# Optimization experiments

Measured on AMD Instinct MI355X. Metric: run time of the kernel, lower is better.

## Reference

```python
import jax, jax.numpy as jnp
import numpy as np

DIM = 2048
N_HEADS = 16
KV_HEADS = 2
HEAD_DIM = DIM // N_HEADS
N_REP = N_HEADS // KV_HEADS
EPS = 1e-6


def rms_norm(x, weight):
    # norm over last dim in float32, cast back (inputs already fp32 here)
    xf = x.astype(jnp.float32)
    n = xf * jax.lax.rsqrt(jnp.mean(xf * xf, axis=-1, keepdims=True) + EPS)
    return (weight * n).astype(x.dtype)


def rotate_half(x):
    x1, x2 = jnp.split(x, 2, axis=-1)
    return jnp.concatenate((-x2, x1), axis=-1)


def apply_rotary(x, cos, sin):
    return x * cos + rotate_half(x) * sin


def setup_inputs() -> dict:
    key = jax.random.key(0)
    ks = jax.random.split(key, 8)
    B, S = 2, 2048
    x = jax.random.normal(ks[0], (B, S, DIM), dtype=jnp.float32)
    cos = jax.random.uniform(ks[1], (1, 1, S, HEAD_DIM), dtype=jnp.float32)
    sin = jax.random.uniform(ks[2], (1, 1, S, HEAD_DIM), dtype=jnp.float32)
    scale = 0.02
    wq = jax.random.normal(ks[3], (N_HEADS * HEAD_DIM, DIM), dtype=jnp.float32) * scale
    wk = jax.random.normal(ks[4], (KV_HEADS * HEAD_DIM, DIM), dtype=jnp.float32) * scale
    wv = jax.random.normal(ks[5], (KV_HEADS * HEAD_DIM, DIM), dtype=jnp.float32) * scale
    wo = jax.random.normal(ks[6], (DIM, N_HEADS * HEAD_DIM), dtype=jnp.float32) * scale
    q_gamma = jnp.ones((HEAD_DIM,), dtype=jnp.float32)
    k_gamma = jnp.ones((HEAD_DIM,), dtype=jnp.float32)
    return {"x": x, "cos": cos, "sin": sin, "wq": wq, "wk": wk, "wv": wv,
            "wo": wo, "q_gamma": q_gamma, "k_gamma": k_gamma,
            "signal_token_num": 256}


def reference(x, cos, sin, wq, wk, wv, wo, q_gamma, k_gamma, signal_token_num):
    B, S, D = x.shape
    p = signal_token_num
    # projections (Linear with no bias: x @ W.T)
    xq = (x @ wq.T).reshape(B, S, N_HEADS, HEAD_DIM)
    xk = (x @ wk.T).reshape(B, S, KV_HEADS, HEAD_DIM)
    xv = (x @ wv.T).reshape(B, S, KV_HEADS, HEAD_DIM)
    # QK RMSNorm per head_dim
    xq = rms_norm(xq, q_gamma)
    xk = rms_norm(xk, k_gamma)
    # repeat kv heads (GQA) then [B,H,S,hd]
    xk = jnp.repeat(xk, N_REP, axis=2)
    xv = jnp.repeat(xv, N_REP, axis=2)
    xq = xq.transpose(0, 2, 1, 3)
    xk = xk.transpose(0, 2, 1, 3)
    xv = xv.transpose(0, 2, 1, 3)
    # rotary: original applies identical cos/sin to [:p] and [p:] slices == full apply
    xq = apply_rotary(xq, cos, sin)
    xk = apply_rotary(xk, cos, sin)
    # causal mask with bidirectional prefix block [:p,:p]
    i = jnp.arange(S)[:, None]
    j = jnp.arange(S)[None, :]
    mask = (j <= i) | ((i < p) & (j < p))  # [S,S] bool
    scale = 1.0 / np.sqrt(HEAD_DIM)
    scores = jnp.einsum('bhqd,bhkd->bhqk', xq, xk) * scale
    scores = jnp.where(mask, scores, jnp.finfo(scores.dtype).min)
    attn = jax.nn.softmax(scores, axis=-1)
    out = jnp.einsum('bhqk,bhkd->bhqd', attn, xv)  # [B,H,S,hd]
    out = out.transpose(0, 2, 1, 3).reshape(B, S, N_HEADS * HEAD_DIM)
    return out @ wo.T
```

## Files before the change

### kernel.cpp

```cpp
#include <hip/hip_runtime.h>
#include <stdint.h>

#define S_LEN 2048
#define DIMM  2048
#define NH    16
#define NKV   2

typedef __attribute__((ext_vector_type(8)))  short s16x8;
typedef __attribute__((ext_vector_type(8)))  unsigned short u16x8;
typedef __attribute__((ext_vector_type(4)))  float f32x4;
typedef __attribute__((ext_vector_type(16))) float f32x16;
typedef __attribute__((ext_vector_type(4)))  unsigned int u32x4;

__device__ __forceinline__ unsigned short f2bf(float f){
  unsigned int u = __builtin_bit_cast(unsigned int, f);
  u += 0x7fffu + ((u >> 16) & 1u);
  return (unsigned short)(u >> 16);
}

__device__ __forceinline__ float bf2f(unsigned short u){
  return __builtin_bit_cast(float, ((unsigned int)u) << 16);
}

__device__ __forceinline__ unsigned int cvtpk(float lo, float hi){
  unsigned int r;
  asm("v_cvt_pk_bf16_f32 %0, %1, %2" : "=v"(r) : "v"(lo), "v"(hi));
  return r;
}

__device__ __forceinline__ void gload16(const void* g, void* l){
  __builtin_amdgcn_global_load_lds(
      (const __attribute__((address_space(1))) unsigned int*)g,
      (__attribute__((address_space(3))) unsigned int*)l, 16, 0, 0);
}

__global__ __launch_bounds__(256) void cvt_all(const float* __restrict__ x,
    const float* __restrict__ wq, const float* __restrict__ wk,
    const float* __restrict__ wv, const float* __restrict__ wo,
    unsigned short* __restrict__ xb, unsigned short* __restrict__ wqkvb,
    unsigned short* __restrict__ wob){
  long gid = (long)blockIdx.x * 256 + threadIdx.x;
  const float* src; unsigned short* dst; long off;
  if (gid < 1048576)      { src = x;  dst = xb;              off = gid; }
  else if (gid < 1572864) { src = wq; dst = wqkvb;           off = gid - 1048576; }
  else if (gid < 1638400) { src = wk; dst = wqkvb + 4194304; off = gid - 1572864; }
  else if (gid < 1703936) { src = wv; dst = wqkvb + 4718592; off = gid - 1638400; }
  else                    { src = wo; dst = wob;             off = gid - 1703936; }
  long i = off * 8;
  const float4* s4 = (const float4*)(src + i);
  float4 a = s4[0], b = s4[1];
  u16x8 o;
  o[0]=f2bf(a.x); o[1]=f2bf(a.y); o[2]=f2bf(a.z); o[3]=f2bf(a.w);
  o[4]=f2bf(b.x); o[5]=f2bf(b.y); o[6]=f2bf(b.z); o[7]=f2bf(b.w);
  *(u16x8*)(dst + i) = o;
}

template<bool OBF16>
__global__ __launch_bounds__(256) void gemm_bt(const unsigned short* __restrict__ A,
                                               const unsigned short* __restrict__ W,
                                               void* __restrict__ Cv,
                                               int M, int N, int K){
  __shared__ __attribute__((aligned(16))) unsigned short As[128*64];
  __shared__ __attribute__((aligned(16))) unsigned short Bs[128*64];
  const int t = threadIdx.x;
  const int lane = t & 63, wave = t >> 6;
  const int l15 = lane & 15, g = lane >> 4;
  const int lid = blockIdx.y * gridDim.x + blockIdx.x;
  const int cpx = (gridDim.x * gridDim.y) >> 3;
  const int swz = (lid & 7) * cpx + (lid >> 3);
  const int m0 = (swz / gridDim.x) * 128, n0 = (swz % gridDim.x) * 128;
  const int wm = (wave >> 1) * 64, wn = (wave & 1) * 64;
  const int srow = t >> 3, sdblk = t & 7;
  const long ldsoff = (long)(t >> 6) * 1024;
  f32x4 acc[4][4] = {};
  for (int k0 = 0; k0 < K; k0 += 64){
    __syncthreads();
    #pragma unroll
    for (int r = 0; r < 4; ++r){
      int row = r*32 + srow;
      int db  = sdblk ^ (row & 7);
      gload16(A + (long)(m0+row)*K + k0 + db*8, (char*)As + r*4096 + ldsoff);
    }
    #pragma unroll
    for (int r = 0; r < 4; ++r){
      int row = r*32 + srow;
      int db  = sdblk ^ (row & 7);
      gload16(W + (long)(n0+row)*K + k0 + db*8, (char*)Bs + r*4096 + ldsoff);
    }
    __syncthreads();
    s16x8 af[4][2], bfr[4][2];
    #pragma unroll
    for (int mi = 0; mi < 4; ++mi)
      #pragma unroll
      for (int kc = 0; kc < 2; ++kc){
        int row = wm + mi*16 + l15;
        int db = (kc*4 + g) ^ (row & 7);
        af[mi][kc] = *(const s16x8*)(As + row*64 + db*8);
      }
    #pragma unroll
    for (int ni = 0; ni < 4; ++ni)
      #pragma unroll
      for (int kc = 0; kc < 2; ++kc){
        int row = wn + ni*16 + l15;
        int db = (kc*4 + g) ^ (row & 7);
        bfr[ni][kc] = *(const s16x8*)(Bs + row*64 + db*8);
      }
    #pragma unroll
    for (int mi = 0; mi < 4; ++mi)
      #pragma unroll
      for (int ni = 0; ni < 4; ++ni)
        #pragma unroll
        for (int kc = 0; kc < 2; ++kc)
          acc[mi][ni] = __builtin_amdgcn_mfma_f32_16x16x32_bf16(af[mi][kc], bfr[ni][kc], acc[mi][ni], 0, 0, 0);
  }
  #pragma unroll
  for (int mi = 0; mi < 4; ++mi)
    #pragma unroll
    for (int ni = 0; ni < 4; ++ni)
      #pragma unroll
      for (int rg = 0; rg < 4; ++rg){
        int row = m0 + wm + mi*16 + g*4 + rg;
        int col = n0 + wn + ni*16 + l15;
        if (OBF16)
          ((unsigned short*)Cv)[(long)row*N + col] = f2bf(acc[mi][ni][rg]);
        else
          ((float*)Cv)[(long)row*N + col] = acc[mi][ni][rg];
      }
}

__global__ __launch_bounds__(256) void normrope(const unsigned short* __restrict__ qkv,
    const float* __restrict__ cosb, const float* __restrict__ sinb,
    const float* __restrict__ qg, const float* __restrict__ kg,
    unsigned short* __restrict__ q_attn, unsigned short* __restrict__ k_attn){
  int wave = threadIdx.x >> 6, lane = threadIdx.x & 63;
  int rid = blockIdx.x * 4 + wave;
  int d0 = lane * 2;
  const unsigned short* src; unsigned short* dst; const float* gm; float sc; int s;
  if (rid < 2*S_LEN*NH){
    int bs = rid >> 4, h = rid & 15;
    int b = bs >> 11; s = bs & 2047;
    src = qkv + (long)bs*2560 + h*128;
    dst = q_attn + ((long)(b*NH + h)*S_LEN + s)*128;
    gm = qg; sc = 0.08838834764831845f * 1.4426950408889634f;
  } else {
    int r2 = rid - 2*S_LEN*NH;
    int bs = r2 >> 1, kv = r2 & 1;
    int b = bs >> 11; s = bs & 2047;
    src = qkv + (long)bs*2560 + 2048 + kv*128;
    dst = k_attn + ((long)(b*NKV + kv)*S_LEN + s)*128;
    gm = kg; sc = 1.0f;
  }
  unsigned int xw = *(const unsigned int*)(src + d0);
  float x0 = bf2f((unsigned short)(xw & 0xffff));
  float x1 = bf2f((unsigned short)(xw >> 16));
  float ss = x0*x0 + x1*x1;
  #pragma unroll
  for (int m = 1; m < 64; m <<= 1) ss += __shfl_xor(ss, m);
  float r = rsqrtf(ss * (1.0f/128.0f) + 1e-6f);
  float2 gv = *(const float2*)(gm + d0);
  float n0 = x0 * r * gv.x, n1 = x1 * r * gv.y;
  float p0 = __shfl_xor(n0, 32), p1 = __shfl_xor(n1, 32);
  float sgn = (d0 < 64) ? -1.f : 1.f;
  float2 c  = *(const float2*)(cosb + (long)s*128 + d0);
  float2 sn = *(const float2*)(sinb + (long)s*128 + d0);
  float o0 = (n0*c.x + sgn*p0*sn.x) * sc;
  float o1 = (n1*c.y + sgn*p1*sn.y) * sc;
  unsigned int pk = (unsigned int)f2bf(o0) | ((unsigned int)f2bf(o1) << 16);
  *(unsigned int*)(dst + d0) = pk;
}

__global__ __launch_bounds__(256) void vtrans(const unsigned short* __restrict__ qkv,
                                              unsigned short* __restrict__ v_t){
  __shared__ __attribute__((aligned(16))) unsigned short lds[128*72];
  int bid = blockIdx.x;
  int s0 = (bid & 31) * 64;
  int kv = (bid >> 5) & 1;
  int b  = bid >> 6;
  int t = threadIdx.x;
  #pragma unroll
  for (int it = 0; it < 32; ++it){
    int idx = it*256 + t;
    int s = idx >> 7, d = idx & 127;
    lds[d*72 + s] = qkv[(long)(b*S_LEN + s0 + s)*2560 + 2304 + kv*128 + d];
  }
  __syncthreads();
  #pragma unroll
  for (int it = 0; it < 4; ++it){
    int c = it*256 + t;
    int d = c >> 3, s8 = c & 7;
    u16x8 vv = *(const u16x8*)(lds + d*72 + s8*8);
    *(u16x8*)(v_t + ((long)(b*NKV + kv)*128 + d)*S_LEN + s0 + s8*8) = vv;
  }
}

__global__ __launch_bounds__(128, 2) void attn_fwd(const unsigned short* __restrict__ q_attn,
    const unsigned short* __restrict__ k_attn, const unsigned short* __restrict__ v_t,
    unsigned short* __restrict__ attn_out, const int* __restrict__ pp){
  __shared__ __attribute__((aligned(16))) unsigned short Ks[2][64*128];
  const int p = pp[0];
  int bid = blockIdx.x;
  int qsb = 31 - (bid >> 5);
  int bh = bid & 31;
  int h = bh & 15, b = bh >> 4;
  int kvh = h >> 3;
  int t = threadIdx.x, wave = t >> 6, lane = t & 63;
  int l31 = lane & 31, hi = lane >> 5;
  int QS = qsb * 64;
  int qw0 = QS + wave*32;
  const int q = qw0 + l31;
  const unsigned short* qb = q_attn + ((long)(b*NH + h)*S_LEN + q)*128 + hi*8;
  s16x8 qf[8];
  #pragma unroll
  for (int m = 0; m < 8; ++m) qf[m] = *(const s16x8*)(qb + m*16);
  f32x16 O[4] = {};
  float mr = -3e38f, lr = 0.f;
  int kvend_w = (qw0 + 31 < p) ? ((p > qw0 + 32) ? p : qw0 + 32) : (qw0 + 32);
  int n_w = (kvend_w + 63) >> 6;
  int kvend_b = (QS + 63 < p) ? ((p > QS + 64) ? p : QS + 64) : (QS + 64);
  int n_blk = (kvend_b + 63) >> 6;
  const unsigned short* kb0 = k_attn + ((long)(b*NKV + kvh)*S_LEN)*128;
  const unsigned short* vb0 = v_t + ((long)(b*NKV + kvh)*128)*S_LEN;
  const int srow8 = t >> 4, sunit = t & 15;
  const long ldsoff = (long)wave * 1024;
  const unsigned short* vbase = vb0 + (long)l31*S_LEN + hi*8;

  #pragma unroll
  for (int r = 0; r < 8; ++r){
    int row = r*8 + srow8;
    int un  = sunit ^ (row & 15);
    gload16(kb0 + (long)row*128 + un*8, (char*)Ks[0] + r*2048 + ldsoff);
  }
  __syncthreads();
  int buf = 0;

  #pragma unroll 1
  for (int ti = 0; ti < n_blk; ++ti){
    int j0 = ti * 64;
    bool act = ti < n_w;
    s16x8 vfA[2][4], vfB[2][4];
    if (act){
      #pragma unroll
      for (int dt = 0; dt < 2; ++dt)
        #pragma unroll
        for (int km = 0; km < 4; ++km)
          vfA[dt][km] = *(const s16x8*)(vbase + (long)dt*32*S_LEN + j0 + km*16);
    }
    if (ti + 1 < n_blk){
      const unsigned short* kb = kb0 + (long)(j0 + 64)*128;
      char* dst = (char*)Ks[buf^1] + ldsoff;
      #pragma unroll
      for (int r = 0; r < 8; ++r){
        int row = r*8 + srow8;
        int un  = sunit ^ (row & 15);
        gload16(kb + (long)row*128 + un*8, dst + r*2048);
      }
    }
    if (act){
      const unsigned short* ksc = Ks[buf];
      f32x16 sa[2] = {};
      __builtin_amdgcn_s_setprio(1);
      #pragma unroll
      for (int kt = 0; kt < 2; ++kt){
        int row = kt*32 + l31;
        #pragma unroll
        for (int m = 0; m < 8; ++m){
          int un = (2*m + hi) ^ (row & 15);
          s16x8 kf = *(const s16x8*)(ksc + row*128 + un*8);
          sa[kt] = __builtin_amdgcn_mfma_f32_32x32x16_bf16(kf, qf[m], sa[kt], 0, 0, 0);
        }
      }
      __builtin_amdgcn_s_setprio(0);
      #pragma unroll
      for (int dt = 0; dt < 2; ++dt)
        #pragma unroll
        for (int km = 0; km < 4; ++km)
          vfB[dt][km] = *(const s16x8*)(vbase + (long)(dt+2)*32*S_LEN + j0 + km*16);
      float tm = -3e38f;
      bool full = (j0 + 63 <= qw0) || ((qw0 + 31 < p) && (j0 + 63 < p));
      if (full){
        #pragma unroll
        for (int kt = 0; kt < 2; ++kt)
          #pragma unroll
          for (int rg = 0; rg < 16; ++rg) tm = fmaxf(tm, sa[kt][rg]);
      } else {
        #pragma unroll
        for (int kt = 0; kt < 2; ++kt)
          #pragma unroll
          for (int rg = 0; rg < 16; ++rg){
            int j = j0 + kt*32 + (rg & 3) + 8*(rg >> 2) + 4*hi;
            bool ok = (j <= q) || ((q < p) && (j < p));
            float sv = ok ? sa[kt][rg] : -3e38f;
            sa[kt][rg] = sv;
            tm = fmaxf(tm, sv);
          }
      }
      tm = fmaxf(tm, __shfl_xor(tm, 32));
      if (!__all(tm <= mr + 8.0f)){
        float nm = fmaxf(mr, tm);
        float sfv = exp2f(mr - nm);
        mr = nm;
        lr *= sfv;
        float sfO[16];
        #pragma unroll
        for (int rg = 0; rg < 16; ++rg){
          int qr = (rg & 3) + 8*(rg >> 2) + 4*hi;
          sfO[rg] = __shfl(sfv, qr | (lane & 32));
        }
        #pragma unroll
        for (int dt = 0; dt < 4; ++dt)
          #pragma unroll
          for (int rg = 0; rg < 16; ++rg) O[dt][rg] *= sfO[rg];
      }
      float rs = 0.f;
      #pragma unroll
      for (int kt = 0; kt < 2; ++kt)
        #pragma unroll
        for (int rg = 0; rg < 16; ++rg){
          float e = exp2f(sa[kt][rg] - mr);
          sa[kt][rg] = e;
          rs += e;
        }
      rs += __shfl_xor(rs, 32);
      lr += rs;
      __builtin_amdgcn_s_setprio(1);
      #pragma unroll
      for (int km = 0; km < 4; ++km){
        int base = (km & 1) * 8;
        const f32x16& s = sa[km >> 1];
        unsigned int a0 = cvtpk(s[base+0], s[base+1]);
        unsigned int b0 = cvtpk(s[base+4], s[base+5]);
        asm("v_permlane32_swap_b32 %0, %1" : "+v"(a0), "+v"(b0));
        unsigned int a1 = cvtpk(s[base+2], s[base+3]);
        unsigned int b1 = cvtpk(s[base+6], s[base+7]);
        asm("v_permlane32_swap_b32 %0, %1" : "+v"(a1), "+v"(b1));
        u32x4 w; w[0] = a0; w[1] = a1; w[2] = b0; w[3] = b1;
        s16x8 pf = __builtin_bit_cast(s16x8, w);
        #pragma unroll
        for (int dt = 0; dt < 2; ++dt)
          O[dt] = __builtin_amdgcn_mfma_f32_32x32x16_bf16(pf, vfA[dt][km], O[dt], 0, 0, 0);
        #pragma unroll
        for (int dt = 2; dt < 4; ++dt)
          O[dt] = __builtin_amdgcn_mfma_f32_32x32x16_bf16(pf, vfB[dt-2][km], O[dt], 0, 0, 0);
      }
      __builtin_amdgcn_s_setprio(0);
    }
    __syncthreads();
    buf ^= 1;
  }
  float inv = 1.0f / lr;
  float invO[16];
  #pragma unroll
  for (int rg = 0; rg < 16; ++rg){
    int qr = (rg & 3) + 8*(rg >> 2) + 4*hi;
    invO[rg] = __shfl(inv, qr | (lane & 32));
  }
  #pragma unroll
  for (int dt = 0; dt < 4; ++dt)
    #pragma unroll
    for (int rg = 0; rg < 16; ++rg){
      int row = qw0 + (rg & 3) + 8*(rg >> 2) + 4*hi;
      int col = h*128 + dt*32 + l31;
      attn_out[(long)(b*S_LEN + row)*DIMM + col] = f2bf(O[dt][rg]*invO[rg]);
    }
}

extern "C" void kernel_launch(void* const* d_in, const int* in_sizes, int n_in,
                              void* d_out, int out_size, void* d_ws, size_t ws_size,
                              hipStream_t stream){
  const float* x    = (const float*)d_in[0];
  const float* cosb = (const float*)d_in[1];
  const float* sinb = (const float*)d_in[2];
  const float* wq   = (const float*)d_in[3];
  const float* wk   = (const float*)d_in[4];
  const float* wv   = (const float*)d_in[5];
  const float* wo   = (const float*)d_in[6];
  const float* qg   = (const float*)d_in[7];
  const float* kg   = (const float*)d_in[8];
  const int*   pp   = (const int*)d_in[9];

  char* ws = (char*)d_ws;
  unsigned short* xb    = (unsigned short*)(ws);
  unsigned short* wqkvb = (unsigned short*)(ws + 16777216);
  unsigned short* wob   = (unsigned short*)(ws + 27262976);
  unsigned short* qkvb  = (unsigned short*)(ws + 35651584);
  unsigned short* qat   = (unsigned short*)(ws + 77594624);
  unsigned short* kat   = (unsigned short*)(ws + 94371840);
  unsigned short* vt    = (unsigned short*)(ws + 96468992);
  unsigned short* aout  = (unsigned short*)(ws + 98566144);

  cvt_all<<<8704, 256, 0, stream>>>(x, wq, wk, wv, wo, xb, wqkvb, wob);

  gemm_bt<true><<<dim3(2560/128, 4096/128), 256, 0, stream>>>(xb, wqkvb, qkvb, 4096, 2560, 2048);
  normrope<<<73728/4, 256, 0, stream>>>(qkvb, cosb, sinb, qg, kg, qat, kat);
  vtrans<<<128, 256, 0, stream>>>(qkvb, vt);
  attn_fwd<<<1024, 128, 0, stream>>>(qat, kat, vt, aout, pp);
  gemm_bt<false><<<dim3(2048/128, 4096/128), 256, 0, stream>>>(aout, wob, d_out, 4096, 2048, 2048);
}
```

Before: 236.4 us.

## Restructure attention to single-wave blocks with 32-key tiles and waitcnt-based sync

The attention kernel now runs one wave per block, with 2048 blocks of 32 queries instead of 1024 blocks of two waves. KV tiles shrink from 64 to 32 keys. Because no LDS tile is shared between waves, __syncthreads is replaced by explicit vmcnt waits, and the per-wave idle iterations in causal tiles are gone. The costs are less K reuse per block (each wave loads its own K), more blocks, and smaller MFMA batches per iteration. The hand-written vmcnt counts are also fragile and depend on the compiler's ordering of loads.

After: 270.2 us. 1.14x slower.

```diff
diff --git a/kernel.cpp b/kernel.cpp
--- a/kernel.cpp
+++ b/kernel.cpp
@@ -193,20 +193,19 @@
   }
 }
 
-__global__ __launch_bounds__(128, 2) void attn_fwd(const unsigned short* __restrict__ q_attn,
+__global__ __launch_bounds__(64) void attn_fwd(const unsigned short* __restrict__ q_attn,
     const unsigned short* __restrict__ k_attn, const unsigned short* __restrict__ v_t,
     unsigned short* __restrict__ attn_out, const int* __restrict__ pp){
-  __shared__ __attribute__((aligned(16))) unsigned short Ks[2][64*128];
+  __shared__ __attribute__((aligned(16))) unsigned short Ks[2][32*128];
   const int p = pp[0];
   int bid = blockIdx.x;
-  int qsb = 31 - (bid >> 5);
+  int qsb = 63 - (bid >> 5);
   int bh = bid & 31;
   int h = bh & 15, b = bh >> 4;
   int kvh = h >> 3;
-  int t = threadIdx.x, wave = t >> 6, lane = t & 63;
+  int lane = threadIdx.x & 63;
   int l31 = lane & 31, hi = lane >> 5;
-  int QS = qsb * 64;
-  int qw0 = QS + wave*32;
+  int qw0 = qsb * 32;
   const int q = qw0 + l31;
   const unsigned short* qb = q_attn + ((long)(b*NH + h)*S_LEN + q)*128 + hi*8;
   s16x8 qf[8];
@@ -214,137 +213,114 @@
   for (int m = 0; m < 8; ++m) qf[m] = *(const s16x8*)(qb + m*16);
   f32x16 O[4] = {};
   float mr = -3e38f, lr = 0.f;
-  int kvend_w = (qw0 + 31 < p) ? ((p > qw0 + 32) ? p : qw0 + 32) : (qw0 + 32);
-  int n_w = (kvend_w + 63) >> 6;
-  int kvend_b = (QS + 63 < p) ? ((p > QS + 64) ? p : QS + 64) : (QS + 64);
-  int n_blk = (kvend_b + 63) >> 6;
+  int kv_end = (qw0 + 31 < p) ? ((p > qw0 + 32) ? p : qw0 + 32) : (qw0 + 32);
+  int n_w = (kv_end + 31) >> 5;
   const unsigned short* kb0 = k_attn + ((long)(b*NKV + kvh)*S_LEN)*128;
   const unsigned short* vb0 = v_t + ((long)(b*NKV + kvh)*128)*S_LEN;
-  const int srow8 = t >> 4, sunit = t & 15;
-  const long ldsoff = (long)wave * 1024;
+  const int srow = lane >> 4, sunit = lane & 15;
   const unsigned short* vbase = vb0 + (long)l31*S_LEN + hi*8;
 
   #pragma unroll
   for (int r = 0; r < 8; ++r){
-    int row = r*8 + srow8;
+    int row = r*4 + srow;
     int un  = sunit ^ (row & 15);
-    gload16(kb0 + (long)row*128 + un*8, (char*)Ks[0] + r*2048 + ldsoff);
-  }
-  __syncthreads();
+    gload16(kb0 + (long)row*128 + un*8, (char*)Ks[0] + r*1024);
+  }
+  asm volatile("s_waitcnt vmcnt(0)" ::: "memory");
+  __builtin_amdgcn_sched_barrier(0);
   int buf = 0;
 
   #pragma unroll 1
-  for (int ti = 0; ti < n_blk; ++ti){
-    int j0 = ti * 64;
-    bool act = ti < n_w;
-    s16x8 vfA[2][4], vfB[2][4];
-    if (act){
-      #pragma unroll
-      for (int dt = 0; dt < 2; ++dt)
+  for (int ti = 0; ti < n_w; ++ti){
+    int j0 = ti * 32;
+    s16x8 vf[4][2];
+    #pragma unroll
+    for (int dt = 0; dt < 4; ++dt)
+      #pragma unroll
+      for (int km = 0; km < 2; ++km)
+        vf[dt][km] = *(const s16x8*)(vbase + (long)dt*32*S_LEN + j0 + km*16);
+    if (ti + 1 < n_w){
+      const unsigned short* kb = kb0 + (long)(j0 + 32)*128;
+      char* dst = (char*)Ks[buf^1];
+      #pragma unroll
+      for (int r = 0; r < 8; ++r){
+        int row = r*4 + srow;
+        int un  = sunit ^ (row & 15);
+        gload16(kb + (long)row*128 + un*8, dst + r*1024);
+      }
+      asm volatile("s_waitcnt vmcnt(16)" ::: "memory");
+    } else {
+      asm volatile("s_waitcnt vmcnt(8)" ::: "memory");
+    }
+    __builtin_amdgcn_sched_barrier(0);
+    const unsigned short* ksc = Ks[buf];
+    f32x16 sa = {};
+    __builtin_amdgcn_s_setprio(1);
+    #pragma unroll
+    for (int m = 0; m < 8; ++m){
+      int un = (2*m + hi) ^ (l31 & 15);
+      s16x8 kf = *(const s16x8*)(ksc + l31*128 + un*8);
+      sa = __builtin_amdgcn_mfma_f32_32x32x16_bf16(kf, qf[m], sa, 0, 0, 0);
+    }
+    __builtin_amdgcn_s_setprio(0);
+    float tm = -3e38f;
+    bool full = (j0 + 31 <= qw0) || ((qw0 + 31 < p) && (j0 + 31 < p));
+    if (full){
+      #pragma unroll
+      for (int rg = 0; rg < 16; ++rg) tm = fmaxf(tm, sa[rg]);
+    } else {
+      #pragma unroll
+      for (int rg = 0; rg < 16; ++rg){
+        int j = j0 + (rg & 3) + 8*(rg >> 2) + 4*hi;
+        bool ok = (j <= q) || ((q < p) && (j < p));
+        float sv = ok ? sa[rg] : -3e38f;
+        sa[rg] = sv;
+        tm = fmaxf(tm, sv);
+      }
+    }
+    tm = fmaxf(tm, __shfl_xor(tm, 32));
+    if (!__all(tm <= mr + 8.0f)){
+      float nm = fmaxf(mr, tm);
+      float sfv = exp2f(mr - nm);
+      mr = nm;
+      lr *= sfv;
+      float sfO[16];
+      #pragma unroll
+      for (int rg = 0; rg < 16; ++rg){
+        int qr = (rg & 3) + 8*(rg >> 2) + 4*hi;
+        sfO[rg] = __shfl(sfv, qr | (lane & 32));
+      }
+      #pragma unroll
+      for (int dt = 0; dt < 4; ++dt)
         #pragma unroll
-        for (int km = 0; km < 4; ++km)
-          vfA[dt][km] = *(const s16x8*)(vbase + (long)dt*32*S_LEN + j0 + km*16);
-    }
-    if (ti + 1 < n_blk){
-      const unsigned short* kb = kb0 + (long)(j0 + 64)*128;
-      char* dst = (char*)Ks[buf^1] + ldsoff;
-      #pragma unroll
-      for (int r = 0; r < 8; ++r){
-        int row = r*8 + srow8;
-        int un  = sunit ^ (row & 15);
-        gload16(kb + (long)row*128 + un*8, dst + r*2048);
-      }
-    }
-    if (act){
-      const unsigned short* ksc = Ks[buf];
-      f32x16 sa[2] = {};
-      __builtin_amdgcn_s_setprio(1);
-      #pragma unroll
-      for (int kt = 0; kt < 2; ++kt){
-        int row = kt*32 + l31;
-        #pragma unroll
-        for (int m = 0; m < 8; ++m){
-          int un = (2*m + hi) ^ (row & 15);
-          s16x8 kf = *(const s16x8*)(ksc + row*128 + un*8);
-          sa[kt] = __builtin_amdgcn_mfma_f32_32x32x16_bf16(kf, qf[m], sa[kt], 0, 0, 0);
-        }
-      }
-      __builtin_amdgcn_s_setprio(0);
-      #pragma unroll
-      for (int dt = 0; dt < 2; ++dt)
-        #pragma unroll
-        for (int km = 0; km < 4; ++km)
-          vfB[dt][km] = *(const s16x8*)(vbase + (long)(dt+2)*32*S_LEN + j0 + km*16);
-      float tm = -3e38f;
-      bool full = (j0 + 63 <= qw0) || ((qw0 + 31 < p) && (j0 + 63 < p));
-      if (full){
-        #pragma unroll
-        for (int kt = 0; kt < 2; ++kt)
-          #pragma unroll
-          for (int rg = 0; rg < 16; ++rg) tm = fmaxf(tm, sa[kt][rg]);
-      } else {
-        #pragma unroll
-        for (int kt = 0; kt < 2; ++kt)
-          #pragma unroll
-          for (int rg = 0; rg < 16; ++rg){
-            int j = j0 + kt*32 + (rg & 3) + 8*(rg >> 2) + 4*hi;
-            bool ok = (j <= q) || ((q < p) && (j < p));
-            float sv = ok ? sa[kt][rg] : -3e38f;
-            sa[kt][rg] = sv;
-            tm = fmaxf(tm, sv);
-          }
-      }
-      tm = fmaxf(tm, __shfl_xor(tm, 32));
-      if (!__all(tm <= mr + 8.0f)){
-        float nm = fmaxf(mr, tm);
-        float sfv = exp2f(mr - nm);
-        mr = nm;
-        lr *= sfv;
-        float sfO[16];
-        #pragma unroll
-        for (int rg = 0; rg < 16; ++rg){
-          int qr = (rg & 3) + 8*(rg >> 2) + 4*hi;
-          sfO[rg] = __shfl(sfv, qr | (lane & 32));
-        }
-        #pragma unroll
-        for (int dt = 0; dt < 4; ++dt)
-          #pragma unroll
-          for (int rg = 0; rg < 16; ++rg) O[dt][rg] *= sfO[rg];
-      }
-      float rs = 0.f;
-      #pragma unroll
-      for (int kt = 0; kt < 2; ++kt)
-        #pragma unroll
-        for (int rg = 0; rg < 16; ++rg){
-          float e = exp2f(sa[kt][rg] - mr);
-          sa[kt][rg] = e;
-          rs += e;
-        }
-      rs += __shfl_xor(rs, 32);
-      lr += rs;
-      __builtin_amdgcn_s_setprio(1);
-      #pragma unroll
-      for (int km = 0; km < 4; ++km){
-        int base = (km & 1) * 8;
-        const f32x16& s = sa[km >> 1];
-        unsigned int a0 = cvtpk(s[base+0], s[base+1]);
-        unsigned int b0 = cvtpk(s[base+4], s[base+5]);
-        asm("v_permlane32_swap_b32 %0, %1" : "+v"(a0), "+v"(b0));
-        unsigned int a1 = cvtpk(s[base+2], s[base+3]);
-        unsigned int b1 = cvtpk(s[base+6], s[base+7]);
-        asm("v_permlane32_swap_b32 %0, %1" : "+v"(a1), "+v"(b1));
-        u32x4 w; w[0] = a0; w[1] = a1; w[2] = b0; w[3] = b1;
-        s16x8 pf = __builtin_bit_cast(s16x8, w);
-        #pragma unroll
-        for (int dt = 0; dt < 2; ++dt)
-          O[dt] = __builtin_amdgcn_mfma_f32_32x32x16_bf16(pf, vfA[dt][km], O[dt], 0, 0, 0);
-        #pragma unroll
-        for (int dt = 2; dt < 4; ++dt)
-          O[dt] = __builtin_amdgcn_mfma_f32_32x32x16_bf16(pf, vfB[dt-2][km], O[dt], 0, 0, 0);
-      }
-      __builtin_amdgcn_s_setprio(0);
-    }
-    __syncthreads();
+        for (int rg = 0; rg < 16; ++rg) O[dt][rg] *= sfO[rg];
+    }
+    float rs = 0.f;
+    #pragma unroll
+    for (int rg = 0; rg < 16; ++rg){
+      float e = exp2f(sa[rg] - mr);
+      sa[rg] = e;
+      rs += e;
+    }
+    rs += __shfl_xor(rs, 32);
+    lr += rs;
+    __builtin_amdgcn_s_setprio(1);
+    #pragma unroll
+    for (int km = 0; km < 2; ++km){
+      int base = km * 8;
+      unsigned int a0 = cvtpk(sa[base+0], sa[base+1]);
+      unsigned int b0 = cvtpk(sa[base+4], sa[base+5]);
+      asm("v_permlane32_swap_b32 %0, %1" : "+v"(a0), "+v"(b0));
+      unsigned int a1 = cvtpk(sa[base+2], sa[base+3]);
+      unsigned int b1 = cvtpk(sa[base+6], sa[base+7]);
+      asm("v_permlane32_swap_b32 %0, %1" : "+v"(a1), "+v"(b1));
+      u32x4 w; w[0] = a0; w[1] = a1; w[2] = b0; w[3] = b1;
+      s16x8 pf = __builtin_bit_cast(s16x8, w);
+      #pragma unroll
+      for (int dt = 0; dt < 4; ++dt)
+        O[dt] = __builtin_amdgcn_mfma_f32_32x32x16_bf16(pf, vf[dt][km], O[dt], 0, 0, 0);
+    }
+    __builtin_amdgcn_s_setprio(0);
     buf ^= 1;
   }
   float inv = 1.0f / lr;
@@ -393,6 +369,6 @@
   gemm_bt<true><<<dim3(2560/128, 4096/128), 256, 0, stream>>>(xb, wqkvb, qkvb, 4096, 2560, 2048);
   normrope<<<73728/4, 256, 0, stream>>>(qkvb, cosb, sinb, qg, kg, qat, kat);
   vtrans<<<128, 256, 0, stream>>>(qkvb, vt);
-  attn_fwd<<<1024, 128, 0, stream>>>(qat, kat, vt, aout, pp);
+  attn_fwd<<<2048, 64, 0, stream>>>(qat, kat, vt, aout, pp);
   gemm_bt<false><<<dim3(2048/128, 4096/128), 256, 0, stream>>>(aout, wob, d_out, 4096, 2048, 2048);
 }
```

## Fuse QK RMSNorm and rotary into the QKV projection GEMM epilogue

Applied to the files above, without the earlier changes.

A dedicated QKV GEMM kernel now applies per-head RMSNorm, gamma, rotary and the softmax scale in its epilogue and writes Q and K directly in attention layout. This removes the separate normrope launch and a full round-trip of Q/K through global memory. Per-row sums of squares are reduced across the two waves of a 128-column tile through shared memory, and the rotary partner value is read from an LDS buffer. V tiles still write to the qkv buffer for vtrans. The epilogue adds extra LDS use, synchronisation and uncoalesced 2-byte stores.

Measured after the change: 293.6 us. 24.2% more time.

```diff
diff --git a/kernel.cpp b/kernel.cpp
--- a/kernel.cpp
+++ b/kernel.cpp
@@ -55,10 +55,155 @@
   *(u16x8*)(dst + i) = o;
 }
 
-template<bool OBF16>
+__global__ __launch_bounds__(256) void gemm_qkv(const unsigned short* __restrict__ A,
+    const unsigned short* __restrict__ W, unsigned short* __restrict__ Cv,
+    const float* __restrict__ cosb, const float* __restrict__ sinb,
+    const float* __restrict__ qg, const float* __restrict__ kg,
+    unsigned short* __restrict__ q_attn, unsigned short* __restrict__ k_attn){
+  __shared__ __attribute__((aligned(16))) char smemraw[34816];
+  unsigned short* As = (unsigned short*)smemraw;
+  unsigned short* Bs = (unsigned short*)(smemraw + 16384);
+  const int N = 2560, K = 2048;
+  const int t = threadIdx.x;
+  const int lane = t & 63, wave = t >> 6;
+  const int l15 = lane & 15, g = lane >> 4;
+  const int lid = blockIdx.y * gridDim.x + blockIdx.x;
+  const int cpx = (gridDim.x * gridDim.y) >> 3;
+  const int swz = (lid & 7) * cpx + (lid >> 3);
+  const int m0 = (swz / gridDim.x) * 128, n0 = (swz % gridDim.x) * 128;
+  const int wm = (wave >> 1) * 64, wn = (wave & 1) * 64;
+  const int srow = t >> 3, sdblk = t & 7;
+  const long ldsoff = (long)(t >> 6) * 1024;
+  f32x4 acc[4][4] = {};
+  for (int k0 = 0; k0 < K; k0 += 64){
+    __syncthreads();
+    #pragma unroll
+    for (int r = 0; r < 4; ++r){
+      int row = r*32 + srow;
+      int db  = sdblk ^ (row & 7);
+      gload16(A + (long)(m0+row)*K + k0 + db*8, (char*)As + r*4096 + ldsoff);
+    }
+    #pragma unroll
+    for (int r = 0; r < 4; ++r){
+      int row = r*32 + srow;
+      int db  = sdblk ^ (row & 7);
+      gload16(W + (long)(n0+row)*K + k0 + db*8, (char*)Bs + r*4096 + ldsoff);
+    }
+    __syncthreads();
+    s16x8 af[4][2], bfr[4][2];
+    #pragma unroll
+    for (int mi = 0; mi < 4; ++mi)
+      #pragma unroll
+      for (int kc = 0; kc < 2; ++kc){
+        int row = wm + mi*16 + l15;
+        int db = (kc*4 + g) ^ (row & 7);
+        af[mi][kc] = *(const s16x8*)(As + row*64 + db*8);
+      }
+    #pragma unroll
+    for (int ni = 0; ni < 4; ++ni)
+      #pragma unroll
+      for (int kc = 0; kc < 2; ++kc){
+        int row = wn + ni*16 + l15;
+        int db = (kc*4 + g) ^ (row & 7);
+        bfr[ni][kc] = *(const s16x8*)(Bs + row*64 + db*8);
+      }
+    #pragma unroll
+    for (int mi = 0; mi < 4; ++mi)
+      #pragma unroll
+      for (int ni = 0; ni < 4; ++ni)
+        #pragma unroll
+        for (int kc = 0; kc < 2; ++kc)
+          acc[mi][ni] = __builtin_amdgcn_mfma_f32_16x16x32_bf16(af[mi][kc], bfr[ni][kc], acc[mi][ni], 0, 0, 0);
+  }
+  if (n0 >= 2304){
+    #pragma unroll
+    for (int mi = 0; mi < 4; ++mi)
+      #pragma unroll
+      for (int ni = 0; ni < 4; ++ni)
+        #pragma unroll
+        for (int rg = 0; rg < 4; ++rg){
+          int row = m0 + wm + mi*16 + g*4 + rg;
+          int col = n0 + wn + ni*16 + l15;
+          Cv[(long)row*N + col] = f2bf(acc[mi][ni][rg]);
+        }
+    return;
+  }
+  __syncthreads();
+  float* ssb = (float*)smemraw;
+  unsigned short* nbuf = (unsigned short*)(smemraw + 1024);
+  float ssp[4][4];
+  #pragma unroll
+  for (int mi = 0; mi < 4; ++mi)
+    #pragma unroll
+    for (int rg = 0; rg < 4; ++rg){
+      float s = 0.f;
+      #pragma unroll
+      for (int ni = 0; ni < 4; ++ni){ float v = acc[mi][ni][rg]; s += v*v; }
+      ssp[mi][rg] = s;
+    }
+  #pragma unroll
+  for (int mk = 1; mk <= 8; mk <<= 1)
+    #pragma unroll
+    for (int mi = 0; mi < 4; ++mi)
+      #pragma unroll
+      for (int rg = 0; rg < 4; ++rg) ssp[mi][rg] += __shfl_xor(ssp[mi][rg], mk);
+  if (l15 == 0){
+    #pragma unroll
+    for (int mi = 0; mi < 4; ++mi)
+      #pragma unroll
+      for (int rg = 0; rg < 4; ++rg)
+        ssb[(wm + mi*16 + g*4 + rg)*2 + (wave & 1)] = ssp[mi][rg];
+  }
+  __syncthreads();
+  const float* gamma = (n0 < 2048) ? qg : kg;
+  #pragma unroll
+  for (int mi = 0; mi < 4; ++mi)
+    #pragma unroll
+    for (int rg = 0; rg < 4; ++rg){
+      int rowl = wm + mi*16 + g*4 + rg;
+      float sum = ssb[rowl*2] + ssb[rowl*2+1];
+      float rms = rsqrtf(sum * (1.0f/128.0f) + 1e-6f);
+      #pragma unroll
+      for (int ni = 0; ni < 4; ++ni){
+        int d = wn + ni*16 + l15;
+        nbuf[rowl*128 + d] = f2bf(acc[mi][ni][rg] * rms * gamma[d]);
+      }
+    }
+  __syncthreads();
+  const float sc = (n0 < 2048) ? (0.08838834764831845f * 1.4426950408889634f) : 1.0f;
+  unsigned short* dst0;
+  if (n0 < 2048){
+    int h = n0 >> 7;
+    dst0 = q_attn + (long)h*S_LEN*128;
+  } else {
+    int kv = (n0 - 2048) >> 7;
+    dst0 = k_attn + (long)kv*S_LEN*128;
+  }
+  const long headstride = (n0 < 2048) ? (long)NH*S_LEN*128 : (long)NKV*S_LEN*128;
+  #pragma unroll
+  for (int mi = 0; mi < 4; ++mi)
+    #pragma unroll
+    for (int rg = 0; rg < 4; ++rg){
+      int rowl = wm + mi*16 + g*4 + rg;
+      int grow = m0 + rowl;
+      int b = grow >> 11, s = grow & 2047;
+      #pragma unroll
+      for (int ni = 0; ni < 4; ++ni){
+        int d = wn + ni*16 + l15;
+        float own = bf2f(nbuf[rowl*128 + d]);
+        float pv  = bf2f(nbuf[rowl*128 + (d ^ 64)]);
+        float c  = cosb[(long)s*128 + d];
+        float sn = sinb[(long)s*128 + d];
+        float sgn = (d < 64) ? -1.f : 1.f;
+        float o = (own*c + sgn*pv*sn) * sc;
+        dst0[b*headstride + ((long)s)*128 + d] = f2bf(o);
+      }
+    }
+}
+
 __global__ __launch_bounds__(256) void gemm_bt(const unsigned short* __restrict__ A,
                                                const unsigned short* __restrict__ W,
-                                               void* __restrict__ Cv,
+                                               float* __restrict__ C,
                                                int M, int N, int K){
   __shared__ __attribute__((aligned(16))) unsigned short As[128*64];
   __shared__ __attribute__((aligned(16))) unsigned short Bs[128*64];
@@ -121,52 +266,8 @@
       for (int rg = 0; rg < 4; ++rg){
         int row = m0 + wm + mi*16 + g*4 + rg;
         int col = n0 + wn + ni*16 + l15;
-        if (OBF16)
-          ((unsigned short*)Cv)[(long)row*N + col] = f2bf(acc[mi][ni][rg]);
-        else
-          ((float*)Cv)[(long)row*N + col] = acc[mi][ni][rg];
-      }
-}
-
-__global__ __launch_bounds__(256) void normrope(const unsigned short* __restrict__ qkv,
-    const float* __restrict__ cosb, const float* __restrict__ sinb,
-    const float* __restrict__ qg, const float* __restrict__ kg,
-    unsigned short* __restrict__ q_attn, unsigned short* __restrict__ k_attn){
-  int wave = threadIdx.x >> 6, lane = threadIdx.x & 63;
-  int rid = blockIdx.x * 4 + wave;
-  int d0 = lane * 2;
-  const unsigned short* src; unsigned short* dst; const float* gm; float sc; int s;
-  if (rid < 2*S_LEN*NH){
-    int bs = rid >> 4, h = rid & 15;
-    int b = bs >> 11; s = bs & 2047;
-    src = qkv + (long)bs*2560 + h*128;
-    dst = q_attn + ((long)(b*NH + h)*S_LEN + s)*128;
-    gm = qg; sc = 0.08838834764831845f * 1.4426950408889634f;
-  } else {
-    int r2 = rid - 2*S_LEN*NH;
-    int bs = r2 >> 1, kv = r2 & 1;
-    int b = bs >> 11; s = bs & 2047;
-    src = qkv + (long)bs*2560 + 2048 + kv*128;
-    dst = k_attn + ((long)(b*NKV + kv)*S_LEN + s)*128;
-    gm = kg; sc = 1.0f;
-  }
-  unsigned int xw = *(const unsigned int*)(src + d0);
-  float x0 = bf2f((unsigned short)(xw & 0xffff));
-  float x1 = bf2f((unsigned short)(xw >> 16));
-  float ss = x0*x0 + x1*x1;
-  #pragma unroll
-  for (int m = 1; m < 64; m <<= 1) ss += __shfl_xor(ss, m);
-  float r = rsqrtf(ss * (1.0f/128.0f) + 1e-6f);
-  float2 gv = *(const float2*)(gm + d0);
-  float n0 = x0 * r * gv.x, n1 = x1 * r * gv.y;
-  float p0 = __shfl_xor(n0, 32), p1 = __shfl_xor(n1, 32);
-  float sgn = (d0 < 64) ? -1.f : 1.f;
-  float2 c  = *(const float2*)(cosb + (long)s*128 + d0);
-  float2 sn = *(const float2*)(sinb + (long)s*128 + d0);
-  float o0 = (n0*c.x + sgn*p0*sn.x) * sc;
-  float o1 = (n1*c.y + sgn*p1*sn.y) * sc;
-  unsigned int pk = (unsigned int)f2bf(o0) | ((unsigned int)f2bf(o1) << 16);
-  *(unsigned int*)(dst + d0) = pk;
+        C[(long)row*N + col] = acc[mi][ni][rg];
+      }
 }
 
 __global__ __launch_bounds__(256) void vtrans(const unsigned short* __restrict__ qkv,
@@ -390,9 +491,9 @@
 
   cvt_all<<<8704, 256, 0, stream>>>(x, wq, wk, wv, wo, xb, wqkvb, wob);
 
-  gemm_bt<true><<<dim3(2560/128, 4096/128), 256, 0, stream>>>(xb, wqkvb, qkvb, 4096, 2560, 2048);
-  normrope<<<73728/4, 256, 0, stream>>>(qkvb, cosb, sinb, qg, kg, qat, kat);
+  gemm_qkv<<<dim3(2560/128, 4096/128), 256, 0, stream>>>(xb, wqkvb, qkvb,
+      cosb, sinb, qg, kg, qat, kat);
   vtrans<<<128, 256, 0, stream>>>(qkvb, vt);
   attn_fwd<<<1024, 128, 0, stream>>>(qat, kat, vt, aout, pp);
-  gemm_bt<false><<<dim3(2048/128, 4096/128), 256, 0, stream>>>(aout, wob, d_out, 4096, 2048, 2048);
-}
+  gemm_bt<<<dim3(2048/128, 4096/128), 256, 0, stream>>>(aout, wob, (float*)d_out, 4096, 2048, 2048);
+}
```
